# Performance work log

Measured on AMD Instinct MI355X. Metric: run time of the kernel, lower is better.

## Reference

```python
import jax, jax.numpy as jnp
import numpy as np

L, B, S, D, H, V = 6, 4, 1024, 1024, 16, 32000
HD = D // H          # head_size = 64
F = 4 * D            # ffn hidden
EPS = 1e-5           # nn.LayerNorm default


def setup_inputs() -> dict:
    key = jax.random.key(0)
    ks = jax.random.split(key, 12)
    s = 0.02
    p = {
        "tokens": jax.random.randint(ks[0], (B, S), 0, V, dtype=jnp.int32),
        "tok_emb": s * jax.random.normal(ks[1], (V, D), jnp.float32),
        "pos_emb": s * jax.random.normal(ks[2], (S, D), jnp.float32),
        # stacked per-layer params (leading dim L)
        "Wq": s * jax.random.normal(ks[3], (L, D, D), jnp.float32),
        "Wk": s * jax.random.normal(ks[4], (L, D, D), jnp.float32),
        "Wv": s * jax.random.normal(ks[5], (L, D, D), jnp.float32),
        "Wp": s * jax.random.normal(ks[6], (L, D, D), jnp.float32),
        "ln1_s": jnp.ones((L, D), jnp.float32),
        "ln1_b": jnp.zeros((L, D), jnp.float32),
        "W1": s * jax.random.normal(ks[7], (L, D, F), jnp.float32),
        "b1": jnp.zeros((L, F), jnp.float32),
        "W2": s * jax.random.normal(ks[8], (L, F, D), jnp.float32),
        "b2": jnp.zeros((L, D), jnp.float32),
        "ln2_s": jnp.ones((L, D), jnp.float32),
        "ln2_b": jnp.zeros((L, D), jnp.float32),
        "lnf_s": jnp.ones((D,), jnp.float32),
        "lnf_b": jnp.zeros((D,), jnp.float32),
        "Wh": s * jax.random.normal(ks[9], (D, V), jnp.float32),
        "bh": jnp.zeros((V,), jnp.float32),
    }
    return p


def _ln(x, scale, bias):
    m = x.mean(-1, keepdims=True)
    v = ((x - m) ** 2).mean(-1, keepdims=True)
    return (x - m) * jax.lax.rsqrt(v + EPS) * scale + bias


def reference(tokens, tok_emb, pos_emb, Wq, Wk, Wv, Wp, ln1_s, ln1_b,
              W1, b1, W2, b2, ln2_s, ln2_b, lnf_s, lnf_b, Wh, bh):
    x = tok_emb[tokens] + pos_emb[None, :, :]            # [B,S,D]
    mask = jnp.tril(jnp.ones((S, S), dtype=bool))
    inv_sqrt_hd = HD ** -0.5

    def layer(x, p):
        wq, wk, wv, wp, l1s, l1b, w1, b1_, w2, b2_, l2s, l2b = p
        q = jnp.einsum('bsd,dhk->bhsk', x, wq.reshape(D, H, HD))
        k = jnp.einsum('bsd,dhk->bhsk', x, wk.reshape(D, H, HD))
        v = jnp.einsum('bsd,dhk->bhsk', x, wv.reshape(D, H, HD))
        scores = jnp.einsum('bhsk,bhtk->bhst', q, k)     # [B,H,S,S]
        # original: masked_fill(-inf) THEN * head_size**-0.5 (same math: -inf stays -inf)
        scores = jnp.where(mask, scores * inv_sqrt_hd, -jnp.inf)
        attn = jax.nn.softmax(scores, axis=-1)
        o = jnp.einsum('bhst,bhtk->bhsk', attn, v)
        o = o.transpose(0, 2, 1, 3).reshape(B, S, D) @ wp
        a = x + _ln(o, l1s, l1b)                          # residual + ln1 (as in source)
        f = jax.nn.relu(a @ w1 + b1_) @ w2 + b2_
        return x + _ln(f, l2s, l2b), None                 # residual from block INPUT (as in source)

    x, _ = jax.lax.scan(layer, x,
                        (Wq, Wk, Wv, Wp, ln1_s, ln1_b, W1, b1, W2, b2, ln2_s, ln2_b))
    return _ln(x, lnf_s, lnf_b) @ Wh + bh                 # [B,S,V]
```

## Files before the change

### kernel.cpp

```cpp
#include <hip/hip_runtime.h>

#define DEV __device__ __forceinline__

typedef __attribute__((ext_vector_type(4))) float f32x4;
typedef __attribute__((ext_vector_type(8))) short short8_t;

constexpr int LNUM = 6;
constexpr int BB = 4;
constexpr int SS = 1024;
constexpr int DD = 1024;
constexpr int HH = 16;
constexpr int HDD = 64;
constexpr int FF = 4096;
constexpr int VV = 32000;
constexpr int MROWS = BB * SS;

DEV short f2bf(float f) {
  union { float f; unsigned u; } x; x.f = f;
  unsigned r = x.u + 0x7fffu + ((x.u >> 16) & 1u);
  return (short)(r >> 16);
}

DEV float bf2f(short s) {
  union { unsigned u; float f; } x;
  x.u = ((unsigned)(unsigned short)s) << 16;
  return x.f;
}

#define BAR() do { __builtin_amdgcn_sched_barrier(0); \
  __builtin_amdgcn_s_barrier(); \
  __builtin_amdgcn_sched_barrier(0); } while (0)

__global__ __launch_bounds__(256) void k_embed(
    const int* __restrict__ tok, const float* __restrict__ te,
    const float* __restrict__ pe, float* __restrict__ xf,
    short* __restrict__ xb) {
  int i = blockIdx.x * 256 + threadIdx.x;
  int bs = i >> 8, d4 = i & 255;
  int t = tok[bs];
  float4 a = ((const float4*)(te + (size_t)t * DD))[d4];
  float4 b = ((const float4*)(pe + (size_t)(bs & (SS - 1)) * DD))[d4];
  float4 r; r.x = a.x + b.x; r.y = a.y + b.y; r.z = a.z + b.z; r.w = a.w + b.w;
  ((float4*)xf)[i] = r;
  short4 o; o.x = f2bf(r.x); o.y = f2bf(r.y); o.z = f2bf(r.z); o.w = f2bf(r.w);
  ((short4*)xb)[i] = o;
}

__global__ __launch_bounds__(256) void k_tcvt4(
    const float* __restrict__ in, short* __restrict__ out, int K, int N,
    long long istride, long long ostride) {
  __shared__ float tile[64][65];
  const float* ip = in + (size_t)blockIdx.z * istride;
  short* op = out + (size_t)blockIdx.z * ostride;
  const int bn = blockIdx.x * 64, bk = blockIdx.y * 64;
  const int tc = threadIdx.x & 15, tr = threadIdx.x >> 4;
  #pragma unroll
  for (int i = 0; i < 4; i++) {
    const int r = tr + 16 * i;
    float4 v = *(const float4*)&ip[(size_t)(bk + r) * N + bn + tc * 4];
    tile[r][tc * 4 + 0] = v.x; tile[r][tc * 4 + 1] = v.y;
    tile[r][tc * 4 + 2] = v.z; tile[r][tc * 4 + 3] = v.w;
  }
  __syncthreads();
  #pragma unroll
  for (int i = 0; i < 4; i++) {
    const int wr = tr + 16 * i;
    short4 s;
    s.x = f2bf(tile[tc * 4 + 0][wr]);
    s.y = f2bf(tile[tc * 4 + 1][wr]);
    s.z = f2bf(tile[tc * 4 + 2][wr]);
    s.w = f2bf(tile[tc * 4 + 3][wr]);
    *(short4*)&op[(size_t)(bn + wr) * K + bk + tc * 4] = s;
  }
}

__global__ __launch_bounds__(256) void k_tcvt4q(
    const float* __restrict__ Wq, const float* __restrict__ Wk,
    const float* __restrict__ Wv, short* __restrict__ out) {
  __shared__ float tile[64][65];
  const int z = blockIdx.z, l = z / 3, which = z - l * 3;
  const float* ip = (which == 0 ? Wq : which == 1 ? Wk : Wv)
                    + (size_t)l * DD * DD;
  short* op = out + (size_t)z * DD * DD;
  const int bn = blockIdx.x * 64, bk = blockIdx.y * 64;
  const int tc = threadIdx.x & 15, tr = threadIdx.x >> 4;
  #pragma unroll
  for (int i = 0; i < 4; i++) {
    const int r = tr + 16 * i;
    float4 v = *(const float4*)&ip[(size_t)(bk + r) * DD + bn + tc * 4];
    tile[r][tc * 4 + 0] = v.x; tile[r][tc * 4 + 1] = v.y;
    tile[r][tc * 4 + 2] = v.z; tile[r][tc * 4 + 3] = v.w;
  }
  __syncthreads();
  #pragma unroll
  for (int i = 0; i < 4; i++) {
    const int wr = tr + 16 * i;
    short4 s;
    s.x = f2bf(tile[tc * 4 + 0][wr]);
    s.y = f2bf(tile[tc * 4 + 1][wr]);
    s.z = f2bf(tile[tc * 4 + 2][wr]);
    s.w = f2bf(tile[tc * 4 + 3][wr]);
    *(short4*)&op[(size_t)(bn + wr) * DD + bk + tc * 4] = s;
  }
}

DEV void gload16(const short* g, short* l) {
  __builtin_amdgcn_global_load_lds(
      (const __attribute__((address_space(1))) void*)g,
      (__attribute__((address_space(3))) void*)l, 16, 0, 0);
}

template<int MODE>
DEV void gemm256_body(short* lds,
    const short* __restrict__ A, const short* __restrict__ Bt,
    const float* __restrict__ bias, void* __restrict__ Cp,
    int M, int N, int K, int lda, int ldb) {
  const int tid = threadIdx.x;
  const int nbx = gridDim.x;
  const int nwg = nbx << 4;
  const int hid = blockIdx.y * nbx + blockIdx.x;
  const int cpx = nwg >> 3;
  const int lid = (hid & 7) * cpx + (hid >> 3);
  const int bx = lid >> 4, by = lid & 15;
  const int n0 = bx * 256, m0 = by * 256;

  const int lane = tid & 63;
  const int wid = tid >> 6;
  const int wm = wid >> 2, wn = wid & 3;
  const int l16 = lane & 15, kg = lane >> 4;
  const int xorv = (l16 & 7) << 4;
  const int cs[2] = { ((kg << 4) ^ xorv) >> 1,
                      ((64 | (kg << 4)) ^ xorv) >> 1 };
  const int rr = tid >> 3;
  const int sce = ((((tid & 7) << 4) ^ ((rr & 7) << 4)) >> 1);
  const int ldst = (tid & ~63) * 8;

  const int NT = K >> 6;

  auto stageA = [&](int t2, int c2) {
    const int k0 = t2 << 6;
    const int base = c2 * 32768;
    #pragma unroll
    for (int h = 0; h < 2; h++)
      #pragma unroll
      for (int li = 0; li < 2; li++)
        gload16(A + (size_t)(m0 + h * 128 + li * 64 + rr) * lda + k0 + sce,
                &lds[base + h * 8192 + li * 4096 + ldst]);
  };
  auto stageB = [&](int t2, int c2) {
    const int k0 = t2 << 6;
    const int base = c2 * 32768 + 16384;
    #pragma unroll
    for (int h = 0; h < 2; h++)
      #pragma unroll
      for (int li = 0; li < 2; li++)
        gload16(Bt + (size_t)(n0 + h * 128 + li * 64 + rr) * ldb + k0 + sce,
                &lds[base + h * 8192 + li * 4096 + ldst]);
  };

  f32x4 acc[8][4];
  #pragma unroll
  for (int mi = 0; mi < 8; mi++)
    #pragma unroll
    for (int ni = 0; ni < 4; ni++)
      #pragma unroll
      for (int j = 0; j < 4; j++) acc[mi][ni][j] = 0.f;

  auto storeQ = [&](int mlo, int nlo) {
    #pragma unroll
    for (int mi = 0; mi < 4; mi++)
      #pragma unroll
      for (int ni = 0; ni < 2; ni++)
        #pragma unroll
        for (int j = 0; j < 4; j++) {
          const int r = m0 + wm * 128 + (mlo + mi) * 16 + kg * 4 + j;
          const int c = n0 + wn * 64 + (nlo + ni) * 16 + l16;
          ((float*)Cp)[(size_t)r * N + c] = acc[mlo + mi][nlo + ni][j] + bias[c];
        }
  };

  stageA(0, 0); stageB(0, 0);
  stageA(1, 1); stageB(1, 1);
  asm volatile("s_waitcnt vmcnt(8)" ::: "memory");
  BAR();

  for (int t = 0; t < NT; t++) {
    const int c = t & 1;
    const int ao = c * 32768 + wm * 8192;
    const int bo = c * 32768 + 16384 + (wn >> 1) * 8192 + (wn & 1) * 4096;
    short8_t a[4][2], b0[2][2], b1[2][2];

    #pragma unroll
    for (int mi = 0; mi < 4; mi++)
      #pragma unroll
      for (int kk = 0; kk < 2; kk++)
        a[mi][kk] = *(const short8_t*)&lds[ao + (mi * 16 + l16) * 64 + cs[kk]];
    #pragma unroll
    for (int ni = 0; ni < 2; ni++)
      #pragma unroll
      for (int kk = 0; kk < 2; kk++)
        b0[ni][kk] = *(const short8_t*)&lds[bo + (ni * 16 + l16) * 64 + cs[kk]];
    BAR();
    __builtin_amdgcn_s_setprio(1);
    #pragma unroll
    for (int mi = 0; mi < 4; mi++)
      #pragma unroll
      for (int ni = 0; ni < 2; ni++)
        #pragma unroll
        for (int kk = 0; kk < 2; kk++)
          acc[mi][ni] = __builtin_amdgcn_mfma_f32_16x16x32_bf16(
              a[mi][kk], b0[ni][kk], acc[mi][ni], 0, 0, 0);
    __builtin_amdgcn_s_setprio(0);
    if (MODE == 9 && t == NT - 1) storeQ(0, 0);
    BAR();

    #pragma unroll
    for (int ni = 0; ni < 2; ni++)
      #pragma unroll
      for (int kk = 0; kk < 2; kk++)
        b1[ni][kk] = *(const short8_t*)&lds[bo + ((ni + 2) * 16 + l16) * 64 + cs[kk]];
    BAR();
    __builtin_amdgcn_s_setprio(1);
    #pragma unroll
    for (int mi = 0; mi < 4; mi++)
      #pragma unroll
      for (int ni = 0; ni < 2; ni++)
        #pragma unroll
        for (int kk = 0; kk < 2; kk++)
          acc[mi][ni + 2] = __builtin_amdgcn_mfma_f32_16x16x32_bf16(
              a[mi][kk], b1[ni][kk], acc[mi][ni + 2], 0, 0, 0);
    __builtin_amdgcn_s_setprio(0);
    if (MODE == 9 && t == NT - 1) storeQ(0, 2);
    BAR();

    #pragma unroll
    for (int mi = 0; mi < 4; mi++)
      #pragma unroll
      for (int kk = 0; kk < 2; kk++)
        a[mi][kk] = *(const short8_t*)&lds[ao + ((mi + 4) * 16 + l16) * 64 + cs[kk]];
    if (t + 2 < NT) stageB(t + 2, c);
    BAR();
    __builtin_amdgcn_s_setprio(1);
    #pragma unroll
    for (int mi = 0; mi < 4; mi++)
      #pragma unroll
      for (int ni = 0; ni < 2; ni++)
        #pragma unroll
        for (int kk = 0; kk < 2; kk++)
          acc[mi + 4][ni + 2] = __builtin_amdgcn_mfma_f32_16x16x32_bf16(
              a[mi][kk], b1[ni][kk], acc[mi + 4][ni + 2], 0, 0, 0);
    __builtin_amdgcn_s_setprio(0);
    if (MODE == 9 && t == NT - 1) storeQ(4, 2);
    BAR();

    if (t + 2 < NT) stageA(t + 2, c);
    BAR();
    __builtin_amdgcn_s_setprio(1);
    #pragma unroll
    for (int mi = 0; mi < 4; mi++)
      #pragma unroll
      for (int ni = 0; ni < 2; ni++)
        #pragma unroll
        for (int kk = 0; kk < 2; kk++)
          acc[mi + 4][ni] = __builtin_amdgcn_mfma_f32_16x16x32_bf16(
              a[mi][kk], b0[ni][kk], acc[mi + 4][ni], 0, 0, 0);
    __builtin_amdgcn_s_setprio(0);
    if (t + 2 < NT) asm volatile("s_waitcnt vmcnt(8)" ::: "memory");
    else            asm volatile("s_waitcnt vmcnt(0)" ::: "memory");
    BAR();
  }

  if (MODE == 9) {
    storeQ(4, 0);
    return;
  }
  #pragma unroll
  for (int mi = 0; mi < 8; mi++) {
    #pragma unroll
    for (int ni = 0; ni < 4; ni++) {
      #pragma unroll
      for (int j = 0; j < 4; j++) {
        const int r = m0 + wm * 128 + mi * 16 + kg * 4 + j;
        const int c = n0 + wn * 64 + ni * 16 + l16;
        const float v = acc[mi][ni][j];
        if (MODE == 6) {
          ((short*)Cp)[(size_t)r * N + c] = f2bf(fmaxf(v + bias[c], 0.f));
        } else if (MODE == 8) {
          int kind = c >> 10, cc = c & 1023;
          int b = r >> 10, s = r & 1023, h = cc >> 6, hd = cc & 63;
          size_t off;
          if (kind < 2)
            off = (size_t)kind * MROWS * DD +
                  (((size_t)(b * HH + h) << 10) + s) * HDD + hd;
          else
            off = (size_t)2 * MROWS * DD +
                  (((size_t)(b * HH + h) * HDD + hd) << 10) + s;
          ((short*)Cp)[off] = f2bf(v);
        }
      }
    }
  }
}

__global__ __launch_bounds__(512, 2) void k_qkv(
    const short* __restrict__ A, const short* __restrict__ Bt,
    const float* __restrict__ bias, void* __restrict__ Cp,
    int M, int N, int K, int lda, int ldb) {
  extern __shared__ short lds[];
  gemm256_body<8>(lds, A, Bt, bias, Cp, M, N, K, lda, ldb);
}
__global__ __launch_bounds__(512, 2) void k_ffn1(
    const short* __restrict__ A, const short* __restrict__ Bt,
    const float* __restrict__ bias, void* __restrict__ Cp,
    int M, int N, int K, int lda, int ldb) {
  extern __shared__ short lds[];
  gemm256_body<6>(lds, A, Bt, bias, Cp, M, N, K, lda, ldb);
}
__global__ __launch_bounds__(512, 2) void k_logits(
    const short* __restrict__ A, const short* __restrict__ Bt,
    const float* __restrict__ bias, void* __restrict__ Cp,
    int M, int N, int K, int lda, int ldb) {
  extern __shared__ short lds[];
  gemm256_body<9>(lds, A, Bt, bias, Cp, M, N, K, lda, ldb);
}

template<int MODE>
DEV void gemm128_body(
    const short* __restrict__ A, const short* __restrict__ Bt,
    const float* __restrict__ bias, void* __restrict__ Cp,
    int M, int N, int K, int lda, int ldb) {
  __shared__ short lA[4096];
  __shared__ short lB[4096];
  const int tid = threadIdx.x;
  const int n0 = blockIdx.x * 128, m0 = blockIdx.y * 128;

  const int lane = tid & 63;
  const int wm = (tid >> 6) >> 1, wn = (tid >> 6) & 1;
  const int l16 = lane & 15, kg = lane >> 4;
  const int srow = tid >> 2, scol = (tid & 3) * 8;
  const int lbase = (tid & ~63) * 8;

  f32x4 acc[4][4];
  #pragma unroll
  for (int a = 0; a < 4; a++)
    #pragma unroll
    for (int b = 0; b < 4; b++)
      #pragma unroll
      for (int j = 0; j < 4; j++) acc[a][b][j] = 0.f;

  for (int k0 = 0; k0 < K; k0 += 32) {
    #pragma unroll
    for (int i = 0; i < 2; i++)
      gload16(A + (size_t)(m0 + i * 64 + srow) * lda + (k0 + scol),
              &lA[i * 2048 + lbase]);
    #pragma unroll
    for (int i = 0; i < 2; i++)
      gload16(Bt + (size_t)(n0 + i * 64 + srow) * ldb + (k0 + scol),
              &lB[i * 2048 + lbase]);
    __syncthreads();
    short8_t af[4], bf[4];
    #pragma unroll
    for (int mi = 0; mi < 4; mi++)
      af[mi] = *(const short8_t*)&lA[(wm * 64 + mi * 16 + l16) * 32 + kg * 8];
    #pragma unroll
    for (int ni = 0; ni < 4; ni++)
      bf[ni] = *(const short8_t*)&lB[(wn * 64 + ni * 16 + l16) * 32 + kg * 8];
    #pragma unroll
    for (int mi = 0; mi < 4; mi++)
      #pragma unroll
      for (int ni = 0; ni < 4; ni++)
        acc[mi][ni] = __builtin_amdgcn_mfma_f32_16x16x32_bf16(
            af[mi], bf[ni], acc[mi][ni], 0, 0, 0);
    __syncthreads();
  }

  #pragma unroll
  for (int mi = 0; mi < 4; mi++) {
    #pragma unroll
    for (int ni = 0; ni < 4; ni++) {
      #pragma unroll
      for (int j = 0; j < 4; j++) {
        const int r = m0 + wm * 64 + mi * 16 + kg * 4 + j;
        const int c = n0 + wn * 64 + ni * 16 + l16;
        const float v = acc[mi][ni][j];
        if (MODE == 15) {
          ((short*)Cp)[(size_t)r * N + c] = f2bf(v);
        } else if (MODE == 17) {
          ((short*)Cp)[(size_t)r * N + c] = f2bf(v + bias[c]);
        }
      }
    }
  }
}

__global__ __launch_bounds__(256) void k_proj(
    const short* __restrict__ A, const short* __restrict__ Bt,
    const float* __restrict__ bias, void* __restrict__ Cp,
    int M, int N, int K, int lda, int ldb) {
  gemm128_body<15>(A, Bt, bias, Cp, M, N, K, lda, ldb);
}
__global__ __launch_bounds__(256) void k_ffn2(
    const short* __restrict__ A, const short* __restrict__ Bt,
    const float* __restrict__ bias, void* __restrict__ Cp,
    int M, int N, int K, int lda, int ldb) {
  gemm128_body<17>(A, Bt, bias, Cp, M, N, K, lda, ldb);
}

#define RDSWZ(arr, r, cb) \
  (*(const short8_t*)&arr[((r) << 6) + ((((cb) ^ (((r) & 7) << 4))) >> 1)])
#define RDSWZ7(arr, r, cb) \
  (*(const short8_t*)&arr[((r) << 7) + ((((cb) ^ (((r) & 7) << 4))) >> 1)])

__global__ __launch_bounds__(512, 2) void k_attn(
    const short* __restrict__ Qg, const short* __restrict__ Kgl,
    const short* __restrict__ Vt, short* __restrict__ Og) {
  extern __shared__ short sm[];
  short* lP = sm + 32768;
  const int tid = threadIdx.x;
  const int z = blockIdx.y;
  const int qb = (z < 32) ? blockIdx.x : 7 - blockIdx.x;
  const int q0 = qb << 7;
  const short* Qp = Qg + ((size_t)z << 16);
  const short* Kp = Kgl + ((size_t)z << 16);
  const short* Vp = Vt + ((size_t)z << 16);
  const int bidx = z >> 4, h = z & 15;
  const int lane = tid & 63, w = tid >> 6;
  const int l16 = lane & 15, kg = lane >> 4;
  const int sr = tid >> 3;
  const int scb = ((((tid & 7) << 4) ^ ((sr & 7) << 4)) >> 1);
  const int vr = tid >> 4;
  const int vcb = ((((tid & 15) << 4) ^ ((vr & 7) << 4)) >> 1);
  const int ldst = (tid & ~63) << 3;

  auto stageK = [&](int kt, int c) {
    const int k0 = kt << 7;
    short* dst = sm + c * 16384;
    #pragma unroll
    for (int i = 0; i < 2; i++)
      gload16(Kp + ((size_t)(k0 + i * 64 + sr) << 6) + scb,
              dst + i * 4096 + ldst);
  };
  auto stageV = [&](int kt, int c) {
    const int k0 = kt << 7;
    short* dst = sm + c * 16384 + 8192;
    #pragma unroll
    for (int i = 0; i < 2; i++)
      gload16(Vp + ((size_t)(i * 32 + vr) << 10) + k0 + vcb,
              dst + i * 4096 + ldst);
  };

  #pragma unroll
  for (int i = 0; i < 2; i++)
    gload16(Qp + ((size_t)(q0 + i * 64 + sr) << 6) + scb,
            sm + 16384 + i * 4096 + ldst);
  __syncthreads();
  short8_t aq[2];
  #pragma unroll
  for (int kk = 0; kk < 2; kk++)
    aq[kk] = RDSWZ((sm + 16384), w * 16 + l16, kk * 64 + kg * 16);
  __syncthreads();

  f32x4 acc_o[4];
  float m_r[4], l_r[4];
  #pragma unroll
  for (int j = 0; j < 4; j++) {
    m_r[j] = -3e38f; l_r[j] = 0.f;
    #pragma unroll
    for (int n2 = 0; n2 < 4; n2++) acc_o[n2][j] = 0.f;
  }

  const float C = 0.125f * 1.44269504f;
  const int nkt = qb + 1;
  stageK(0, 0); stageV(0, 0);

  for (int kt = 0; kt < nkt; kt++) {
    const int cur = kt & 1;
    if (kt + 1 < nkt) {
      stageK(kt + 1, cur ^ 1); stageV(kt + 1, cur ^ 1);
      asm volatile("s_waitcnt vmcnt(4)" ::: "memory");
    } else {
      asm volatile("s_waitcnt vmcnt(0)" ::: "memory");
    }
    BAR();

    const short* lK = sm + cur * 16384;
    const short* lV = sm + cur * 16384 + 8192;
    const int k0 = kt << 7;

    f32x4 s[8];
    #pragma unroll
    for (int nf = 0; nf < 8; nf++)
      #pragma unroll
      for (int j = 0; j < 4; j++) s[nf][j] = 0.f;
    #pragma unroll
    for (int kk = 0; kk < 2; kk++)
      #pragma unroll
      for (int nf = 0; nf < 8; nf++) {
        short8_t bk = RDSWZ(lK, nf * 16 + l16, kk * 64 + kg * 16);
        s[nf] = __builtin_amdgcn_mfma_f32_16x16x32_bf16(aq[kk], bk, s[nf], 0, 0, 0);
      }

    const bool diag = (kt == qb);
    #pragma unroll
    for (int j = 0; j < 4; j++) {
      const int ql = w * 16 + kg * 4 + j;
      const int q = q0 + ql;
      float sv[8]; float tm = -3e38f;
      #pragma unroll
      for (int nf = 0; nf < 8; nf++) {
        const int kv = k0 + nf * 16 + l16;
        const float x = s[nf][j] * C;
        sv[nf] = (!diag || kv <= q) ? x : -3e38f;
        tm = fmaxf(tm, sv[nf]);
      }
      #pragma unroll
      for (int o = 1; o < 16; o <<= 1) tm = fmaxf(tm, __shfl_xor(tm, o));
      const float mn = fmaxf(m_r[j], tm);
      const float scale = exp2f(m_r[j] - mn);
      float ts = 0.f;
      #pragma unroll
      for (int nf = 0; nf < 8; nf++) {
        const float e = exp2f(sv[nf] - mn);
        ts += e;
        lP[(ql << 7) + ((nf * 16 + l16) ^ ((ql & 7) << 3))] = f2bf(e);
      }
      #pragma unroll
      for (int o = 1; o < 16; o <<= 1) ts += __shfl_xor(ts, o);
      l_r[j] = l_r[j] * scale + ts;
      m_r[j] = mn;
      #pragma unroll
      for (int n2 = 0; n2 < 4; n2++) acc_o[n2][j] *= scale;
    }

    #pragma unroll
    for (int kc = 0; kc < 4; kc++) {
      const int pr = w * 16 + l16;
      short8_t pa = *(const short8_t*)
          &lP[(pr << 7) + ((kc * 32 + kg * 8) ^ ((pr & 7) << 3))];
      #pragma unroll
      for (int n2 = 0; n2 < 4; n2++) {
        short8_t vb = RDSWZ7(lV, n2 * 16 + l16, kc * 64 + kg * 16);
        acc_o[n2] = __builtin_amdgcn_mfma_f32_16x16x32_bf16(pa, vb, acc_o[n2], 0, 0, 0);
      }
    }
    BAR();
  }

  #pragma unroll
  for (int j = 0; j < 4; j++) {
    const int q = q0 + w * 16 + kg * 4 + j;
    const float inv = 1.f / l_r[j];
    #pragma unroll
    for (int n2 = 0; n2 < 4; n2++) {
      const int col = h * HDD + n2 * 16 + l16;
      Og[(((size_t)bidx << 10) + q) * DD + col] = f2bf(acc_o[n2][j] * inv);
    }
  }
}

template<int SRCB16, int ADD_RES, int WRITE_F32>
__global__ __launch_bounds__(256) void k_ln(
    const void* __restrict__ src, const float* __restrict__ res,
    const float* __restrict__ g, const float* __restrict__ b,
    float* __restrict__ of, short* __restrict__ ob) {
  const int row = blockIdx.x;
  const int tid = threadIdx.x;
  float4 v;
  if (SRCB16) {
    short4 s = ((const short4*)src)[((size_t)row << 8) + tid];
    v.x = bf2f(s.x); v.y = bf2f(s.y); v.z = bf2f(s.z); v.w = bf2f(s.w);
  } else {
    v = ((const float4*)src)[((size_t)row << 8) + tid];
  }
  float s1 = v.x + v.y + v.z + v.w;
  float s2 = v.x * v.x + v.y * v.y + v.z * v.z + v.w * v.w;
  #pragma unroll
  for (int o = 32; o; o >>= 1) { s1 += __shfl_xor(s1, o); s2 += __shfl_xor(s2, o); }
  __shared__ float sh1[4], sh2[4];
  if ((tid & 63) == 0) { sh1[tid >> 6] = s1; sh2[tid >> 6] = s2; }
  __syncthreads();
  s1 = sh1[0] + sh1[1] + sh1[2] + sh1[3];
  s2 = sh2[0] + sh2[1] + sh2[2] + sh2[3];
  const float mean = s1 * (1.f / 1024.f);
  const float var  = s2 * (1.f / 1024.f) - mean * mean;
  const float rs = rsqrtf(var + 1e-5f);
  float4 gg = ((const float4*)g)[tid];
  float4 bb = ((const float4*)b)[tid];
  float4 o4;
  o4.x = (v.x - mean) * rs * gg.x + bb.x;
  o4.y = (v.y - mean) * rs * gg.y + bb.y;
  o4.z = (v.z - mean) * rs * gg.z + bb.z;
  o4.w = (v.w - mean) * rs * gg.w + bb.w;
  if (ADD_RES) {
    float4 rr = ((const float4*)(res + ((size_t)row << 10)))[tid];
    o4.x += rr.x; o4.y += rr.y; o4.z += rr.z; o4.w += rr.w;
  }
  if (WRITE_F32) ((float4*)(of + ((size_t)row << 10)))[tid] = o4;
  short4 s4; s4.x = f2bf(o4.x); s4.y = f2bf(o4.y);
  s4.z = f2bf(o4.z); s4.w = f2bf(o4.w);
  ((short4*)ob)[((size_t)row << 8) + tid] = s4;
}

extern "C" void kernel_launch(void* const* d_in, const int* in_sizes, int n_in,
                              void* d_out, int out_size, void* d_ws, size_t ws_size,
                              hipStream_t stream) {
  (void)in_sizes; (void)n_in; (void)out_size; (void)ws_size;
  const int*   tokens  = (const int*)d_in[0];
  const float* tok_emb = (const float*)d_in[1];
  const float* pos_emb = (const float*)d_in[2];
  const float* Wq = (const float*)d_in[3];
  const float* Wk = (const float*)d_in[4];
  const float* Wv = (const float*)d_in[5];
  const float* Wp = (const float*)d_in[6];
  const float* ln1s = (const float*)d_in[7];
  const float* ln1b = (const float*)d_in[8];
  const float* W1 = (const float*)d_in[9];
  const float* b1 = (const float*)d_in[10];
  const float* W2 = (const float*)d_in[11];
  const float* b2 = (const float*)d_in[12];
  const float* ln2s = (const float*)d_in[13];
  const float* ln2b = (const float*)d_in[14];
  const float* lnfs = (const float*)d_in[15];
  const float* lnfb = (const float*)d_in[16];
  const float* Wh = (const float*)d_in[17];
  const float* bh = (const float*)d_in[18];
  float* out = (float*)d_out;

  hipFuncSetAttribute((const void*)k_qkv,
      hipFuncAttributeMaxDynamicSharedMemorySize, 131072);
  hipFuncSetAttribute((const void*)k_ffn1,
      hipFuncAttributeMaxDynamicSharedMemorySize, 131072);
  hipFuncSetAttribute((const void*)k_logits,
      hipFuncAttributeMaxDynamicSharedMemorySize, 131072);
  hipFuncSetAttribute((const void*)k_attn,
      hipFuncAttributeMaxDynamicSharedMemorySize, 98304);

  char* p = (char*)d_ws;
  auto alloc = [&](size_t elems, size_t esz) -> char* {
    char* r = p; p += (elems * esz + 255) & ~(size_t)255; return r;
  };
  short* WqkvT = (short*)alloc((size_t)LNUM * 3 * DD * DD, 2);
  short* WpT = (short*)alloc((size_t)LNUM * DD * DD, 2);
  short* W1T = (short*)alloc((size_t)LNUM * DD * FF, 2);
  short* W2T = (short*)alloc((size_t)LNUM * DD * FF, 2);
  short* WhT = (short*)alloc((size_t)DD * VV, 2);
  float* xf   = (float*)alloc((size_t)MROWS * DD, 4);
  short* ffb  = (short*)alloc((size_t)MROWS * DD, 2);
  short* xb   = (short*)alloc((size_t)MROWS * DD, 2);
  short* ab   = (short*)alloc((size_t)MROWS * DD, 2);
  short* qkvb = (short*)alloc((size_t)3 * MROWS * DD, 2);
  short* obuf = (short*)alloc((size_t)MROWS * DD, 2);
  short* hb   = (short*)alloc((size_t)MROWS * FF, 2);
  short* xfb  = (short*)alloc((size_t)MROWS * DD, 2);
  short* qb   = qkvb;
  short* kb   = qkvb + (size_t)MROWS * DD;
  short* vtb  = qkvb + (size_t)2 * MROWS * DD;

  dim3 blk(256);
  const long long DD2 = (long long)DD * DD;
  const long long DF  = (long long)DD * FF;
  k_tcvt4q<<<dim3(16, 16, 3 * LNUM), blk, 0, stream>>>(Wq, Wk, Wv, WqkvT);
  k_tcvt4<<<dim3(16, 16, LNUM), blk, 0, stream>>>(Wp, WpT, DD, DD, DD2, DD2);
  k_tcvt4<<<dim3(64, 16, LNUM), blk, 0, stream>>>(W1, W1T, DD, FF, DF, DF);
  k_tcvt4<<<dim3(16, 64, LNUM), blk, 0, stream>>>(W2, W2T, FF, DD, DF, DF);
  k_tcvt4<<<dim3(500, 16, 1),  blk, 0, stream>>>(Wh, WhT, DD, VV, 0, 0);

  k_embed<<<(MROWS * DD / 4) / 256, blk, 0, stream>>>(tokens, tok_emb, pos_emb, xf, xb);

  for (int l = 0; l < LNUM; l++) {
    const short* wqkv = WqkvT + (size_t)l * 3 * DD * DD;
    const short* wp = WpT + (size_t)l * DD * DD;
    const short* w1 = W1T + (size_t)l * DD * FF;
    const short* w2 = W2T + (size_t)l * DD * FF;

    k_qkv<<<dim3(12, 16), 512, 131072, stream>>>(xb, wqkv, nullptr, qkvb,
        MROWS, 3 * DD, DD, DD, DD);
    k_attn<<<dim3(8, BB * HH), 512, 98304, stream>>>(qb, kb, vtb, obuf);
    k_proj<<<dim3(8, 32), blk, 0, stream>>>(obuf, wp, nullptr, ffb,
        MROWS, DD, DD, DD, DD);
    k_ln<1, 1, 0><<<MROWS, blk, 0, stream>>>(ffb, xf, ln1s + (size_t)l * DD,
        ln1b + (size_t)l * DD, nullptr, ab);
    k_ffn1<<<dim3(16, 16), 512, 131072, stream>>>(ab, w1, b1 + (size_t)l * FF, hb,
        MROWS, FF, DD, DD, DD);
    k_ffn2<<<dim3(8, 32), blk, 0, stream>>>(hb, w2, b2 + (size_t)l * DD, ffb,
        MROWS, DD, FF, FF, FF);
    k_ln<1, 1, 1><<<MROWS, blk, 0, stream>>>(ffb, xf, ln2s + (size_t)l * DD,
        ln2b + (size_t)l * DD, xf, xb);
  }

  k_ln<0, 0, 0><<<MROWS, blk, 0, stream>>>(xf, nullptr, lnfs, lnfb, nullptr, xfb);
  k_logits<<<dim3(VV / 256, 16), 512, 131072, stream>>>(xfb, WhT, bh, out,
      MROWS, VV, DD, DD, DD);
}
```

Before: 2.303 ms.

## Double-buffer and swizzle LDS in 128x128 GEMM for proj and ffn2

Rewrites the 128x128 GEMM used by the attention projection and FFN2. It now uses dynamic LDS with two 64-wide K stages, so the next tile's global loads overlap the current MFMAs. It also XOR-swizzles LDS rows to avoid bank conflicts, halves barrier count per K, and raises MFMA wave priority. The cost is 64KB of LDS per block, which may limit occupancy, along with more registers for the fragments.

New measurement: 2.010 ms. 1.15x faster.

```diff
diff --git a/kernel.cpp b/kernel.cpp
--- a/kernel.cpp
+++ b/kernel.cpp
@@ -325,20 +325,37 @@
 }
 
 template<int MODE>
-DEV void gemm128_body(
+DEV void gemm128db_body(short* lds,
     const short* __restrict__ A, const short* __restrict__ Bt,
     const float* __restrict__ bias, void* __restrict__ Cp,
     int M, int N, int K, int lda, int ldb) {
-  __shared__ short lA[4096];
-  __shared__ short lB[4096];
   const int tid = threadIdx.x;
   const int n0 = blockIdx.x * 128, m0 = blockIdx.y * 128;
-
   const int lane = tid & 63;
-  const int wm = (tid >> 6) >> 1, wn = (tid >> 6) & 1;
+  const int wid = tid >> 6;
+  const int wm = wid >> 1, wn = wid & 1;
   const int l16 = lane & 15, kg = lane >> 4;
-  const int srow = tid >> 2, scol = (tid & 3) * 8;
-  const int lbase = (tid & ~63) * 8;
+  const int xorv = (l16 & 7) << 4;
+  const int cs[2] = { ((kg << 4) ^ xorv) >> 1,
+                      ((64 | (kg << 4)) ^ xorv) >> 1 };
+  const int rr = tid >> 3;
+  const int sce = ((((tid & 7) << 4) ^ ((rr & 7) << 4)) >> 1);
+  const int ldst = (tid & ~63) * 8;
+
+  const int NT = K >> 6;
+
+  auto stage = [&](int t2, int c2) {
+    const int k0 = t2 << 6;
+    const int base = c2 * 16384;
+    #pragma unroll
+    for (int i = 0; i < 4; i++)
+      gload16(A + (size_t)(m0 + i * 32 + rr) * lda + k0 + sce,
+              &lds[base + i * 2048 + ldst]);
+    #pragma unroll
+    for (int i = 0; i < 4; i++)
+      gload16(Bt + (size_t)(n0 + i * 32 + rr) * ldb + k0 + sce,
+              &lds[base + 8192 + i * 2048 + ldst]);
+  };
 
   f32x4 acc[4][4];
   #pragma unroll
@@ -348,30 +365,39 @@
       #pragma unroll
       for (int j = 0; j < 4; j++) acc[a][b][j] = 0.f;
 
-  for (int k0 = 0; k0 < K; k0 += 32) {
-    #pragma unroll
-    for (int i = 0; i < 2; i++)
-      gload16(A + (size_t)(m0 + i * 64 + srow) * lda + (k0 + scol),
-              &lA[i * 2048 + lbase]);
-    #pragma unroll
-    for (int i = 0; i < 2; i++)
-      gload16(Bt + (size_t)(n0 + i * 64 + srow) * ldb + (k0 + scol),
-              &lB[i * 2048 + lbase]);
-    __syncthreads();
-    short8_t af[4], bf[4];
-    #pragma unroll
-    for (int mi = 0; mi < 4; mi++)
-      af[mi] = *(const short8_t*)&lA[(wm * 64 + mi * 16 + l16) * 32 + kg * 8];
+  stage(0, 0);
+  asm volatile("s_waitcnt vmcnt(0)" ::: "memory");
+  BAR();
+
+  for (int t = 0; t < NT; t++) {
+    const int c = t & 1;
+    if (t + 1 < NT) stage(t + 1, c ^ 1);
+    const int ab = c * 16384;
+    short8_t a[4][2], b[4][2];
+    #pragma unroll
+    for (int mi = 0; mi < 4; mi++)
+      #pragma unroll
+      for (int kk = 0; kk < 2; kk++)
+        a[mi][kk] = *(const short8_t*)
+            &lds[ab + (wm * 64 + mi * 16 + l16) * 64 + cs[kk]];
     #pragma unroll
     for (int ni = 0; ni < 4; ni++)
-      bf[ni] = *(const short8_t*)&lB[(wn * 64 + ni * 16 + l16) * 32 + kg * 8];
+      #pragma unroll
+      for (int kk = 0; kk < 2; kk++)
+        b[ni][kk] = *(const short8_t*)
+            &lds[ab + 8192 + (wn * 64 + ni * 16 + l16) * 64 + cs[kk]];
+    __builtin_amdgcn_s_setprio(1);
     #pragma unroll
     for (int mi = 0; mi < 4; mi++)
       #pragma unroll
       for (int ni = 0; ni < 4; ni++)
-        acc[mi][ni] = __builtin_amdgcn_mfma_f32_16x16x32_bf16(
-            af[mi], bf[ni], acc[mi][ni], 0, 0, 0);
-    __syncthreads();
+        #pragma unroll
+        for (int kk = 0; kk < 2; kk++)
+          acc[mi][ni] = __builtin_amdgcn_mfma_f32_16x16x32_bf16(
+              a[mi][kk], b[ni][kk], acc[mi][ni], 0, 0, 0);
+    __builtin_amdgcn_s_setprio(0);
+    if (t + 1 < NT) asm volatile("s_waitcnt vmcnt(0)" ::: "memory");
+    BAR();
   }
 
   #pragma unroll
@@ -393,17 +419,19 @@
   }
 }
 
-__global__ __launch_bounds__(256) void k_proj(
+__global__ __launch_bounds__(256, 2) void k_proj(
     const short* __restrict__ A, const short* __restrict__ Bt,
     const float* __restrict__ bias, void* __restrict__ Cp,
     int M, int N, int K, int lda, int ldb) {
-  gemm128_body<15>(A, Bt, bias, Cp, M, N, K, lda, ldb);
-}
-__global__ __launch_bounds__(256) void k_ffn2(
+  extern __shared__ short lds[];
+  gemm128db_body<15>(lds, A, Bt, bias, Cp, M, N, K, lda, ldb);
+}
+__global__ __launch_bounds__(256, 2) void k_ffn2(
     const short* __restrict__ A, const short* __restrict__ Bt,
     const float* __restrict__ bias, void* __restrict__ Cp,
     int M, int N, int K, int lda, int ldb) {
-  gemm128_body<17>(A, Bt, bias, Cp, M, N, K, lda, ldb);
+  extern __shared__ short lds[];
+  gemm128db_body<17>(lds, A, Bt, bias, Cp, M, N, K, lda, ldb);
 }
 
 #define RDSWZ(arr, r, cb) \
@@ -632,6 +660,10 @@
       hipFuncAttributeMaxDynamicSharedMemorySize, 131072);
   hipFuncSetAttribute((const void*)k_logits,
       hipFuncAttributeMaxDynamicSharedMemorySize, 131072);
+  hipFuncSetAttribute((const void*)k_proj,
+      hipFuncAttributeMaxDynamicSharedMemorySize, 65536);
+  hipFuncSetAttribute((const void*)k_ffn2,
+      hipFuncAttributeMaxDynamicSharedMemorySize, 65536);
   hipFuncSetAttribute((const void*)k_attn,
       hipFuncAttributeMaxDynamicSharedMemorySize, 98304);
 
@@ -676,13 +708,13 @@
     k_qkv<<<dim3(12, 16), 512, 131072, stream>>>(xb, wqkv, nullptr, qkvb,
         MROWS, 3 * DD, DD, DD, DD);
     k_attn<<<dim3(8, BB * HH), 512, 98304, stream>>>(qb, kb, vtb, obuf);
-    k_proj<<<dim3(8, 32), blk, 0, stream>>>(obuf, wp, nullptr, ffb,
+    k_proj<<<dim3(8, 32), blk, 65536, stream>>>(obuf, wp, nullptr, ffb,
         MROWS, DD, DD, DD, DD);
     k_ln<1, 1, 0><<<MROWS, blk, 0, stream>>>(ffb, xf, ln1s + (size_t)l * DD,
         ln1b + (size_t)l * DD, nullptr, ab);
     k_ffn1<<<dim3(16, 16), 512, 131072, stream>>>(ab, w1, b1 + (size_t)l * FF, hb,
         MROWS, FF, DD, DD, DD);
-    k_ffn2<<<dim3(8, 32), blk, 0, stream>>>(hb, w2, b2 + (size_t)l * DD, ffb,
+    k_ffn2<<<dim3(8, 32), blk, 65536, stream>>>(hb, w2, b2 + (size_t)l * DD, ffb,
         MROWS, DD, FF, FF, FF);
     k_ln<1, 1, 1><<<MROWS, blk, 0, stream>>>(ffb, xf, ln2s + (size_t)l * DD,
         ln2b + (size_t)l * DD, xf, xb);
```
